# Performance work log

Measured on AMD Instinct MI355X. Metric: run time of the kernel, lower is better.

The kernel has to match this reference:

```python
import jax, jax.numpy as jnp
import numpy as np

N, E, G = 50000, 800000, 64
NODE_IN, EDGE_DIM = 128, 16
H1, C1 = 4, 16            # layer1: 4 heads, 16 ch -> concat 64
H2, C2 = 1, 64            # layer2: 1 head, 64 ch, no concat
OUT = 64


def setup_inputs() -> dict:
    key = jax.random.key(0)
    ks = jax.random.split(key, 20)
    s = 0.05
    inp = {
        "x": jax.random.normal(ks[0], (N, NODE_IN), jnp.float32),
        "edge_index": jax.random.randint(ks[1], (2, E), 0, N, jnp.int32),
        "edge_attr": jax.random.normal(ks[2], (E, EDGE_DIM), jnp.float32),
        "batch": jnp.sort(jax.random.randint(ks[3], (N,), 0, G, jnp.int32)),
        # layer 1 params
        "W1": jax.random.normal(ks[4], (NODE_IN, H1 * C1), jnp.float32) * s,
        "as1": jax.random.normal(ks[5], (H1, C1), jnp.float32) * s,
        "ad1": jax.random.normal(ks[6], (H1, C1), jnp.float32) * s,
        "We1": jax.random.normal(ks[7], (EDGE_DIM, H1 * C1), jnp.float32) * s,
        "ae1": jax.random.normal(ks[8], (H1, C1), jnp.float32) * s,
        "b1": jnp.zeros((H1 * C1,), jnp.float32),
        # layer 2 params
        "W2": jax.random.normal(ks[9], (H1 * C1, H2 * C2), jnp.float32) * s,
        "as2": jax.random.normal(ks[10], (H2, C2), jnp.float32) * s,
        "ad2": jax.random.normal(ks[11], (H2, C2), jnp.float32) * s,
        "We2": jax.random.normal(ks[12], (EDGE_DIM, H2 * C2), jnp.float32) * s,
        "ae2": jax.random.normal(ks[13], (H2, C2), jnp.float32) * s,
        "b2": jnp.zeros((C2,), jnp.float32),
        # final projection
        "Pw": jax.random.normal(ks[14], (OUT, OUT), jnp.float32) * s,
        "Pb": jnp.zeros((OUT,), jnp.float32),
    }
    return inp


def _gat(x, src, dst, edge_attr, W, a_s, a_d, We, a_e, b, heads, ch, concat):
    """PyG GATConv: shared lin, edge features, self-loops with mean fill,
    LeakyReLU(0.2), segment softmax over dst, sum aggregation."""
    n = x.shape[0]
    h = (x @ W).reshape(n, heads, ch)                    # [N,H,C]
    al_s = jnp.einsum("nhc,hc->nh", h, a_s)              # [N,H]
    al_d = jnp.einsum("nhc,hc->nh", h, a_d)
    # add self-loops; loop edge_attr = mean of incoming edge attrs (fill='mean')
    deg = jax.ops.segment_sum(jnp.ones((src.shape[0],), x.dtype), dst, n)
    loop_attr = jax.ops.segment_sum(edge_attr, dst, n) / jnp.maximum(deg, 1.0)[:, None]
    ar = jnp.arange(n, dtype=src.dtype)
    s_idx = jnp.concatenate([src, ar])
    d_idx = jnp.concatenate([dst, ar])
    ea = jnp.concatenate([edge_attr, loop_attr], axis=0)
    al_e = jnp.einsum("ehc,hc->eh", (ea @ We).reshape(-1, heads, ch), a_e)
    alpha = jax.nn.leaky_relu(al_s[s_idx] + al_d[d_idx] + al_e, 0.2)  # [E',H]
    # segment softmax over incoming edges of each dst node
    amax = jax.ops.segment_max(alpha, d_idx, num_segments=n)
    ex = jnp.exp(alpha - amax[d_idx])
    denom = jax.ops.segment_sum(ex, d_idx, num_segments=n)
    att = ex / denom[d_idx]                              # safe: self-loops guarantee denom>0
    msg = h[s_idx] * att[..., None]                      # [E',H,C]
    out = jax.ops.segment_sum(msg.reshape(-1, heads * ch), d_idx, num_segments=n)
    out = out if concat else out.reshape(n, heads, ch).mean(axis=1)
    return out + b


def reference(x, edge_index, edge_attr, batch,
              W1, as1, ad1, We1, ae1, b1,
              W2, as2, ad2, We2, ae2, b2, Pw, Pb):
    src, dst = edge_index[0], edge_index[1]
    h = jax.nn.elu(_gat(x, src, dst, edge_attr, W1, as1, ad1, We1, ae1, b1, H1, C1, True))
    h = _gat(h, src, dst, edge_attr, W2, as2, ad2, We2, ae2, b2, H2, C2, False)
    # global mean pool over graphs
    cnt = jax.ops.segment_sum(jnp.ones((N,), h.dtype), batch, num_segments=G)
    pooled = jax.ops.segment_sum(h, batch, num_segments=G) / jnp.maximum(cnt, 1.0)[:, None]
    return pooled @ Pw + Pb
```

## Files before the change

kernel.cpp:

```cpp
#include <hip/hip_runtime.h>

#define LRELU(a) ((a) > 0.f ? (a) : 0.2f * (a))

__device__ __forceinline__ int blockScanIncl256(int v, int* wl) {
  int t = threadIdx.x, lane = t & 63, w = t >> 6;
  int x = v;
#pragma unroll
  for (int o = 1; o < 64; o <<= 1) {
    int tmp = __shfl_up(x, (unsigned)o, 64);
    if (lane >= o) x += tmp;
  }
  if (lane == 63) wl[w] = x;
  __syncthreads();
  if (t == 0) {
    int s = 0;
#pragma unroll
    for (int j = 0; j < 4; ++j) { int tv = wl[j]; wl[j] = s; s += tv; }
  }
  __syncthreads();
  return x + wl[w];
}

__global__ __launch_bounds__(256) void k_deg(const int* __restrict__ dst,
                                             int* __restrict__ deg, int E) {
  int e = blockIdx.x * 256 + threadIdx.x;
  if (e < E) atomicAdd(&deg[dst[e]], 1);
}

__global__ __launch_bounds__(256) void k_chunksum(const int* __restrict__ deg,
                                                  int* __restrict__ bsum, int n) {
  __shared__ int wl[4];
  int i = blockIdx.x * 256 + threadIdx.x;
  int v = (i < n) ? deg[i] : 0;
#pragma unroll
  for (int o = 1; o < 64; o <<= 1) v += __shfl_xor(v, o, 64);
  int lane = threadIdx.x & 63, w = threadIdx.x >> 6;
  if (lane == 0) wl[w] = v;
  __syncthreads();
  if (threadIdx.x == 0) bsum[blockIdx.x] = wl[0] + wl[1] + wl[2] + wl[3];
}

__global__ __launch_bounds__(256) void k_bscan(int* __restrict__ bsum, int nb,
                                               int* __restrict__ csr_off, int n) {
  __shared__ int wl[4];
  int t = threadIdx.x;
  int v = (t < nb) ? bsum[t] : 0;
  int incl = blockScanIncl256(v, wl);
  if (t < nb) bsum[t] = incl - v;
  if (t == 255) csr_off[n] = incl;
}

__global__ __launch_bounds__(256) void k_chunkscan(const int* __restrict__ deg,
                                                   const int* __restrict__ bsum,
                                                   int* __restrict__ csr_off,
                                                   int* __restrict__ fill, int n) {
  __shared__ int wl[4];
  int i = blockIdx.x * 256 + threadIdx.x;
  int v = (i < n) ? deg[i] : 0;
  int incl = blockScanIncl256(v, wl);
  int o = bsum[blockIdx.x] + incl - v;
  if (i < n) { csr_off[i] = o; fill[i] = o; }
}

template <int K, int HH>
__device__ __forceinline__ void gemm_body(const float* __restrict__ X,
                                          const float* __restrict__ W,
                                          const float* __restrict__ a_s,
                                          const float* __restrict__ a_d,
                                          float* __restrict__ H,
                                          float* __restrict__ als,
                                          float* __restrict__ ald,
                                          int n, int bid) {
  constexpr int KC = 32;
  __shared__ float Xs[64][KC + 4];
  __shared__ float Ws[KC][64 + 4];
  int t = threadIdx.x;
  int b0 = bid * 64;
  int tx = t & 15, ty = t >> 4;
  float acc[4][4] = {};
  for (int kc = 0; kc < K; kc += KC) {
    if (kc) __syncthreads();
    {
      int i = t * 8;
      int node = i >> 5, k = i & 31;
      int r = b0 + node;
      float4 v0 = make_float4(0.f, 0.f, 0.f, 0.f), v1 = v0;
      if (r < n) {
        const float* src = X + (size_t)r * K + kc + k;
        v0 = *(const float4*)src;
        v1 = *(const float4*)(src + 4);
      }
      *(float4*)&Xs[node][k] = v0;
      *(float4*)&Xs[node][k + 4] = v1;
    }
    {
      int i = t * 8;
      int kk = i >> 6, c = i & 63;
      const float* src = W + (size_t)(kc + kk) * 64 + c;
      *(float4*)&Ws[kk][c] = *(const float4*)src;
      *(float4*)&Ws[kk][c + 4] = *(const float4*)(src + 4);
    }
    __syncthreads();
#pragma unroll
    for (int k4 = 0; k4 < KC; k4 += 4) {
      float wvf[4][4];
#pragma unroll
      for (int j = 0; j < 4; ++j)
        *(float4*)&wvf[j][0] = *(const float4*)&Ws[k4 + j][tx * 4];
#pragma unroll
      for (int i = 0; i < 4; ++i) {
        float xvf[4];
        *(float4*)&xvf[0] = *(const float4*)&Xs[ty * 4 + i][k4];
#pragma unroll
        for (int kk = 0; kk < 4; ++kk)
#pragma unroll
          for (int j = 0; j < 4; ++j)
            acc[i][j] = fmaf(xvf[kk], wvf[kk][j], acc[i][j]);
      }
    }
  }
#pragma unroll
  for (int i = 0; i < 4; ++i) {
    int node = b0 + ty * 4 + i;
    if (node < n)
      *(float4*)&H[(size_t)node * 64 + tx * 4] =
          make_float4(acc[i][0], acc[i][1], acc[i][2], acc[i][3]);
  }
  constexpr int C = 64 / HH;
  constexpr int GL = C / 4;
  float asv[4], adv[4];
#pragma unroll
  for (int j = 0; j < 4; ++j) { asv[j] = a_s[tx * 4 + j]; adv[j] = a_d[tx * 4 + j]; }
#pragma unroll
  for (int i = 0; i < 4; ++i) {
    float ps = 0.f, pd = 0.f;
#pragma unroll
    for (int j = 0; j < 4; ++j) {
      ps = fmaf(acc[i][j], asv[j], ps);
      pd = fmaf(acc[i][j], adv[j], pd);
    }
#pragma unroll
    for (int o = 1; o < GL; o <<= 1) {
      ps += __shfl_xor(ps, o, 64);
      pd += __shfl_xor(pd, o, 64);
    }
    int node = b0 + ty * 4 + i;
    if (node < n && (tx & (GL - 1)) == 0) {
      int head = tx / GL;
      als[(size_t)node * HH + head] = ps;
      ald[(size_t)node * HH + head] = pd;
    }
  }
}

__global__ __launch_bounds__(256) void k_gemm2(const float* __restrict__ X,
                                               const float* __restrict__ W,
                                               const float* __restrict__ a_s,
                                               const float* __restrict__ a_d,
                                               float* __restrict__ H,
                                               float* __restrict__ als,
                                               float* __restrict__ ald, int n) {
  gemm_body<64, 1>(X, W, a_s, a_d, H, als, ald, n, blockIdx.x);
}

__global__ __launch_bounds__(256) void k_gs(const float* __restrict__ X,
                                            const float* __restrict__ W,
                                            const float* __restrict__ a_s,
                                            const float* __restrict__ a_d,
                                            float* __restrict__ H,
                                            float* __restrict__ als,
                                            float* __restrict__ ald, int n,
                                            int gemmBlocks,
                                            const int* __restrict__ dst,
                                            const int* __restrict__ src,
                                            const float* __restrict__ edge_attr,
                                            const float* __restrict__ We1,
                                            const float* __restrict__ ae1,
                                            const float* __restrict__ We2,
                                            const float* __restrict__ ae2,
                                            int* __restrict__ fill,
                                            float* __restrict__ epk, int E) {
  if ((int)blockIdx.x < gemmBlocks) {
    gemm_body<128, 4>(X, W, a_s, a_d, H, als, ald, n, blockIdx.x);
  } else {
    __shared__ float wa1s[64];
    __shared__ float wa2s[16];
    int t = threadIdx.x;
    if (t < 64) {
      int k = t >> 2, hh = t & 3;
      float s = 0.f;
#pragma unroll
      for (int c = 0; c < 16; ++c)
        s = fmaf(We1[k * 64 + hh * 16 + c], ae1[hh * 16 + c], s);
      wa1s[t] = s;
    } else if (t < 80) {
      int k = t - 64;
      float s = 0.f;
#pragma unroll
      for (int c = 0; c < 64; ++c) s = fmaf(We2[k * 64 + c], ae2[c], s);
      wa2s[k] = s;
    }
    __syncthreads();
    int base = (blockIdx.x - gemmBlocks) * 512 + t;
#pragma unroll
    for (int r = 0; r < 2; ++r) {
      int e = base + r * 256;
      if (e < E) {
        int d = dst[e], s = src[e];
        const float4* ea = (const float4*)(edge_attr + (size_t)e * 16);
        float ev[16];
        *(float4*)&ev[0]  = ea[0];
        *(float4*)&ev[4]  = ea[1];
        *(float4*)&ev[8]  = ea[2];
        *(float4*)&ev[12] = ea[3];
        float d0 = 0.f, d1 = 0.f, d2 = 0.f, d3 = 0.f, q = 0.f;
#pragma unroll
        for (int k = 0; k < 16; ++k) {
          float4 w1 = *(const float4*)&wa1s[k * 4];
          d0 = fmaf(ev[k], w1.x, d0);
          d1 = fmaf(ev[k], w1.y, d1);
          d2 = fmaf(ev[k], w1.z, d2);
          d3 = fmaf(ev[k], w1.w, d3);
          q  = fmaf(ev[k], wa2s[k], q);
        }
        int p = atomicAdd(&fill[d], 1);
        float* o = epk + (size_t)p * 8;
        *(float4*)o = make_float4(d0, d1, d2, d3);
        *(float4*)(o + 4) = make_float4(q, __int_as_float(s), 0.f, 0.f);
      }
    }
  }
}

__global__ __launch_bounds__(256) void k_agg1(const int* __restrict__ csr_off,
                                              const float* __restrict__ epk,
                                              const float* __restrict__ als1,
                                              const float* __restrict__ ald1,
                                              const float* __restrict__ h1,
                                              const float* __restrict__ b1,
                                              float* __restrict__ out1,
                                              float* __restrict__ loopdot2, int n) {
  int t = threadIdx.x, w = t >> 6, lane = t & 63;
  int node = blockIdx.x * 4 + w;
  if (node >= n) return;
  int s0 = csr_off[node], s1 = csr_off[node + 1];
  int nit = s1 - s0;
  int laneB = lane >> 2, laneH = lane & 3;
  float adv = ald1[(size_t)node * 4 + laneH];
  float m = -3e38f, den = 0.f, sumd = 0.f, sumq = 0.f;
  for (int i = s0 + laneB; i < s1; i += 16) {
    float d = epk[(size_t)i * 8 + laneH];
    int s = __float_as_int(epk[(size_t)i * 8 + 5]);
    float q = epk[(size_t)i * 8 + 4];
    float a = als1[(size_t)s * 4 + laneH] + adv + d;
    a = LRELU(a);
    float nm = fmaxf(m, a);
    den = den * __expf(m - nm) + __expf(a - nm);
    m = nm;
    sumd += d;
    if (laneH == 0) sumq += q;
  }
#pragma unroll
  for (int o = 4; o < 64; o <<= 1) {
    float om = __shfl_xor(m, o, 64);
    float od = __shfl_xor(den, o, 64);
    float nm = fmaxf(m, om);
    den = den * __expf(m - nm) + od * __expf(om - nm);
    m = nm;
    sumd += __shfl_xor(sumd, o, 64);
    sumq += __shfl_xor(sumq, o, 64);
  }
  float cd = fmaxf((float)nit, 1.f);
  float sl = als1[(size_t)node * 4 + laneH] + adv + sumd / cd;
  sl = LRELU(sl);
  {
    float nm = fmaxf(m, sl);
    den = den * __expf(m - nm) + __expf(sl - nm);
    m = nm;
  }
  if (lane == 0) loopdot2[node] = sumq / cd;
  int head = lane >> 4;
  float m_ch = __shfl(m, head, 64);
  float rd_ch = 1.f / __shfl(den, head, 64);
  float sl_ch = __shfl(sl, head, 64);
  float acc = __expf(sl_ch - m_ch) * h1[(size_t)node * 64 + lane];
  float adv_h = __shfl(adv, head, 64);
  if (nit > 0) {
    int nb = (nit + 7) >> 3;
    int laneE = lane & 7, laneB8 = (lane >> 2) & 7;
    int sv; float ev;
    float bufA[8], bufB[8];
    {
      int i1 = min(s0 + laneE, s1 - 1);
      sv = __float_as_int(epk[(size_t)i1 * 8 + 5]);
      int i2 = min(s0 + laneB8, s1 - 1);
      float d = epk[(size_t)i2 * 8 + laneH];
      int se = __float_as_int(epk[(size_t)i2 * 8 + 5]);
      ev = als1[(size_t)se * 4 + laneH] + adv + d;
      ev = LRELU(ev);
    }
#pragma unroll
    for (int j = 0; j < 8; ++j)
      bufA[j] = h1[(size_t)__shfl(sv, j, 64) * 64 + lane];
    for (int b = 0; b < nb; ++b) {
      int svN = 0; float evN = 0.f;
      bool pf = (b + 1 < nb);
      if (pf) {
        int base = s0 + (b + 1) * 8;
        int i1 = min(base + laneE, s1 - 1);
        svN = __float_as_int(epk[(size_t)i1 * 8 + 5]);
        int i2 = min(base + laneB8, s1 - 1);
        float d = epk[(size_t)i2 * 8 + laneH];
        int se = __float_as_int(epk[(size_t)i2 * 8 + 5]);
        evN = als1[(size_t)se * 4 + laneH] + adv + d;
        evN = LRELU(evN);
#pragma unroll
        for (int j = 0; j < 8; ++j)
          bufB[j] = h1[(size_t)__shfl(svN, j, 64) * 64 + lane];
      }
      int rem = nit - b * 8;
#pragma unroll
      for (int j = 0; j < 8; ++j) {
        float aj = __shfl(ev, j * 4 + head, 64);
        float ex = (j < rem) ? __expf(aj - m_ch) : 0.f;
        acc = fmaf(ex, bufA[j], acc);
      }
      if (pf) {
#pragma unroll
        for (int j = 0; j < 8; ++j) bufA[j] = bufB[j];
        sv = svN; ev = evN;
      }
    }
  }
  float r = acc * rd_ch + b1[lane];
  out1[(size_t)node * 64 + lane] = r > 0.f ? r : expm1f(r);
  (void)adv_h;
}

__global__ __launch_bounds__(256) void k_agg2(const int* __restrict__ csr_off,
                                              const float* __restrict__ epk,
                                              const float* __restrict__ als2,
                                              const float* __restrict__ ald2,
                                              const float* __restrict__ loopdot2,
                                              const float* __restrict__ h2,
                                              const float* __restrict__ b2,
                                              float* __restrict__ out2, int n) {
  int t = threadIdx.x, w = t >> 6, lane = t & 63;
  int node = blockIdx.x * 4 + w;
  if (node >= n) return;
  int s0 = csr_off[node], s1 = csr_off[node + 1];
  int nit = s1 - s0;
  float adv = ald2[node];
  float m = -3e38f, den = 0.f;
  for (int i = s0 + lane; i < s1; i += 64) {
    float q = epk[(size_t)i * 8 + 4];
    int s = __float_as_int(epk[(size_t)i * 8 + 5]);
    float a = als2[s] + adv + q;
    a = LRELU(a);
    float nm = fmaxf(m, a);
    den = den * __expf(m - nm) + __expf(a - nm);
    m = nm;
  }
#pragma unroll
  for (int o = 1; o < 64; o <<= 1) {
    float om = __shfl_xor(m, o, 64);
    float od = __shfl_xor(den, o, 64);
    float nm = fmaxf(m, om);
    den = den * __expf(m - nm) + od * __expf(om - nm);
    m = nm;
  }
  float sl = als2[node] + adv + loopdot2[node];
  sl = LRELU(sl);
  {
    float nm = fmaxf(m, sl);
    den = den * __expf(m - nm) + __expf(sl - nm);
    m = nm;
  }
  float rd = 1.f / den;
  float acc = __expf(sl - m) * h2[(size_t)node * 64 + lane];
  if (nit > 0) {
    int nb = (nit + 7) >> 3;
    int laneE = lane & 7;
    int sv; float ev;
    {
      int i1 = min(s0 + laneE, s1 - 1);
      float q = epk[(size_t)i1 * 8 + 4];
      sv = __float_as_int(epk[(size_t)i1 * 8 + 5]);
      ev = LRELU(als2[sv] + adv + q);
    }
    float bufA[8], bufB[8];
#pragma unroll
    for (int j = 0; j < 8; ++j)
      bufA[j] = h2[(size_t)__shfl(sv, j, 64) * 64 + lane];
    for (int b = 0; b < nb; ++b) {
      int svN = 0; float evN = 0.f;
      bool pf = (b + 1 < nb);
      if (pf) {
        int i1 = min(s0 + (b + 1) * 8 + laneE, s1 - 1);
        float q = epk[(size_t)i1 * 8 + 4];
        svN = __float_as_int(epk[(size_t)i1 * 8 + 5]);
        evN = LRELU(als2[svN] + adv + q);
#pragma unroll
        for (int j = 0; j < 8; ++j)
          bufB[j] = h2[(size_t)__shfl(svN, j, 64) * 64 + lane];
      }
      int rem = nit - b * 8;
#pragma unroll
      for (int j = 0; j < 8; ++j) {
        float aj = __shfl(ev, j, 64);
        float ex = (j < rem) ? __expf(aj - m) : 0.f;
        acc = fmaf(ex, bufA[j], acc);
      }
      if (pf) {
#pragma unroll
        for (int j = 0; j < 8; ++j) bufA[j] = bufB[j];
        sv = svN; ev = evN;
      }
    }
  }
  out2[(size_t)node * 64 + lane] = acc * rd + b2[lane];
}

__global__ __launch_bounds__(256) void k_pool(const float* __restrict__ out2,
                                              const int* __restrict__ batch,
                                              float* __restrict__ pooled,
                                              float* __restrict__ cnt, int n) {
  int wgl = blockIdx.x * 4 + (threadIdx.x >> 6);
  int lane = threadIdx.x & 63;
  int i0 = wgl * 64;
  if (i0 >= n) return;
  int i1 = min(i0 + 64, n);
  int cur = -1;
  float acc = 0.f, c = 0.f;
  for (int i = i0; i < i1; ++i) {
    int g = batch[i];
    if (g != cur) {
      if (cur >= 0) {
        atomicAdd(&pooled[cur * 64 + lane], acc);
        if (lane == 0) atomicAdd(&cnt[cur], c);
      }
      cur = g; acc = 0.f; c = 0.f;
    }
    acc += out2[(size_t)i * 64 + lane];
    c += 1.f;
  }
  if (cur >= 0) {
    atomicAdd(&pooled[cur * 64 + lane], acc);
    if (lane == 0) atomicAdd(&cnt[cur], c);
  }
}

__global__ __launch_bounds__(64) void k_final(const float* __restrict__ pooled,
                                              const float* __restrict__ cnt,
                                              const float* __restrict__ Pw,
                                              const float* __restrict__ Pb,
                                              float* __restrict__ out) {
  __shared__ float m[64];
  int g = blockIdx.x, o = threadIdx.x;
  m[o] = pooled[g * 64 + o] / fmaxf(cnt[g], 1.f);
  __syncthreads();
  float s = Pb[o];
#pragma unroll
  for (int c = 0; c < 64; ++c) s = fmaf(m[c], Pw[c * 64 + o], s);
  out[g * 64 + o] = s;
}

extern "C" void kernel_launch(void* const* d_in, const int* in_sizes, int n_in,
                              void* d_out, int out_size, void* d_ws, size_t ws_size,
                              hipStream_t stream) {
  const float* x         = (const float*)d_in[0];
  const int*   edge_index= (const int*)d_in[1];
  const float* edge_attr = (const float*)d_in[2];
  const int*   batch     = (const int*)d_in[3];
  const float* W1  = (const float*)d_in[4];
  const float* as1 = (const float*)d_in[5];
  const float* ad1 = (const float*)d_in[6];
  const float* We1 = (const float*)d_in[7];
  const float* ae1 = (const float*)d_in[8];
  const float* b1  = (const float*)d_in[9];
  const float* W2  = (const float*)d_in[10];
  const float* as2 = (const float*)d_in[11];
  const float* ad2 = (const float*)d_in[12];
  const float* We2 = (const float*)d_in[13];
  const float* ae2 = (const float*)d_in[14];
  const float* b2  = (const float*)d_in[15];
  const float* Pw  = (const float*)d_in[16];
  const float* Pb  = (const float*)d_in[17];

  const int N = in_sizes[0] / 128;
  const int E = in_sizes[1] / 2;
  const int G = out_size / 64;
  const int* srcI = edge_index;
  const int* dstI = edge_index + E;

  float* ws = (float*)d_ws;
  size_t off = 0;
  auto alloc = [&](size_t elems) {
    float* p = ws + off;
    off += (elems + 7) & ~(size_t)7;
    return p;
  };
  int*   deg       = (int*)alloc(N);
  float* cnt       = alloc(G);
  float* pooled    = alloc((size_t)G * 64);
  size_t zero_bytes = off * sizeof(float);
  int*   csr_off   = (int*)alloc(N + 1);
  int*   fill      = (int*)alloc(N);
  int*   bsum      = (int*)alloc(1024);
  float* epk       = alloc((size_t)E * 8);
  float* loopdot2  = alloc((size_t)N);
  float* h         = alloc((size_t)N * 64);
  float* als       = alloc((size_t)N * 4);
  float* ald       = alloc((size_t)N * 4);
  float* outn      = alloc((size_t)N * 64);

  (void)ws_size; (void)n_in;
  hipMemsetAsync(d_ws, 0, zero_bytes, stream);

  const int ebl   = (E + 255) / 256;
  const int nb    = (N + 255) / 256;
  const int nbl4  = (N + 3) / 4;
  const int gemb  = (N + 63) / 64;
  const int sctb  = (E + 511) / 512;

  k_deg<<<ebl, 256, 0, stream>>>(dstI, deg, E);
  k_chunksum<<<nb, 256, 0, stream>>>(deg, bsum, N);
  k_bscan<<<1, 256, 0, stream>>>(bsum, nb, csr_off, N);
  k_chunkscan<<<nb, 256, 0, stream>>>(deg, bsum, csr_off, fill, N);

  k_gs<<<gemb + sctb, 256, 0, stream>>>(x, W1, as1, ad1, h, als, ald, N, gemb,
                                        dstI, srcI, edge_attr, We1, ae1, We2, ae2,
                                        fill, epk, E);

  k_agg1<<<nbl4, 256, 0, stream>>>(csr_off, epk, als, ald, h, b1, outn, loopdot2, N);

  k_gemm2<<<gemb, 256, 0, stream>>>(outn, W2, as2, ad2, h, als, ald, N);
  k_agg2<<<nbl4, 256, 0, stream>>>(csr_off, epk, als, ald, loopdot2, h, b2, outn, N);

  k_pool<<<((N + 63) / 64 + 3) / 4, 256, 0, stream>>>(outn, batch, pooled, cnt, N);
  k_final<<<G, 64, 0, stream>>>(pooled, cnt, Pw, Pb, (float*)d_out);
}
```

Before: 244.1 us.

## Fuse layer-2 linear projection and attention logits into layer-1 aggregation kernel

Layer 1's aggregation kernel now applies ELU, multiplies the 64-wide row by W2 using wavefront shuffles, and writes h2 plus the layer-2 source and destination attention scalars directly. This removes the separate GEMM launch and the round trip of the N x 64 layer-1 output through global memory. It also doubles the edges handled per scatter block and reads the packed q/src pair with a single float2 load in the layer-2 aggregation. In exchange each wavefront runs 64 shuffle-broadcast FMAs that reload W2 from global memory or cache, which adds latency at the tail of the aggregation kernel.

Measured after the change: 261.9 us. 1.07x slower.

```diff
diff --git a/kernel.cpp b/kernel.cpp
--- a/kernel.cpp
+++ b/kernel.cpp
@@ -153,16 +153,6 @@
   }
 }
 
-__global__ __launch_bounds__(256) void k_gemm2(const float* __restrict__ X,
-                                               const float* __restrict__ W,
-                                               const float* __restrict__ a_s,
-                                               const float* __restrict__ a_d,
-                                               float* __restrict__ H,
-                                               float* __restrict__ als,
-                                               float* __restrict__ ald, int n) {
-  gemm_body<64, 1>(X, W, a_s, a_d, H, als, ald, n, blockIdx.x);
-}
-
 __global__ __launch_bounds__(256) void k_gs(const float* __restrict__ X,
                                             const float* __restrict__ W,
                                             const float* __restrict__ a_s,
@@ -201,9 +191,9 @@
       wa2s[k] = s;
     }
     __syncthreads();
-    int base = (blockIdx.x - gemmBlocks) * 512 + t;
-#pragma unroll
-    for (int r = 0; r < 2; ++r) {
+    int base = (blockIdx.x - gemmBlocks) * 1024 + t;
+#pragma unroll
+    for (int r = 0; r < 4; ++r) {
       int e = base + r * 256;
       if (e < E) {
         int d = dst[e], s = src[e];
@@ -238,7 +228,12 @@
                                               const float* __restrict__ ald1,
                                               const float* __restrict__ h1,
                                               const float* __restrict__ b1,
-                                              float* __restrict__ out1,
+                                              const float* __restrict__ W2,
+                                              const float* __restrict__ as2,
+                                              const float* __restrict__ ad2,
+                                              float* __restrict__ h2,
+                                              float* __restrict__ als2,
+                                              float* __restrict__ ald2,
                                               float* __restrict__ loopdot2, int n) {
   int t = threadIdx.x, w = t >> 6, lane = t & 63;
   int node = blockIdx.x * 4 + w;
@@ -284,7 +279,6 @@
   float rd_ch = 1.f / __shfl(den, head, 64);
   float sl_ch = __shfl(sl, head, 64);
   float acc = __expf(sl_ch - m_ch) * h1[(size_t)node * 64 + lane];
-  float adv_h = __shfl(adv, head, 64);
   if (nit > 0) {
     int nb = (nit + 7) >> 3;
     int laneE = lane & 7, laneB8 = (lane >> 2) & 7;
@@ -333,8 +327,28 @@
     }
   }
   float r = acc * rd_ch + b1[lane];
-  out1[(size_t)node * 64 + lane] = r > 0.f ? r : expm1f(r);
-  (void)adv_h;
+  r = r > 0.f ? r : expm1f(r);
+  float a0 = 0.f, a1 = 0.f, a2 = 0.f, a3 = 0.f;
+#pragma unroll
+  for (int k = 0; k < 64; k += 4) {
+    float r0 = __shfl(r, k, 64);
+    float r1 = __shfl(r, k + 1, 64);
+    float r2 = __shfl(r, k + 2, 64);
+    float r3 = __shfl(r, k + 3, 64);
+    a0 = fmaf(r0, W2[(k + 0) * 64 + lane], a0);
+    a1 = fmaf(r1, W2[(k + 1) * 64 + lane], a1);
+    a2 = fmaf(r2, W2[(k + 2) * 64 + lane], a2);
+    a3 = fmaf(r3, W2[(k + 3) * 64 + lane], a3);
+  }
+  float h2v = (a0 + a1) + (a2 + a3);
+  h2[(size_t)node * 64 + lane] = h2v;
+  float ps = h2v * as2[lane], pd = h2v * ad2[lane];
+#pragma unroll
+  for (int o = 1; o < 64; o <<= 1) {
+    ps += __shfl_xor(ps, o, 64);
+    pd += __shfl_xor(pd, o, 64);
+  }
+  if (lane == 0) { als2[node] = ps; ald2[node] = pd; }
 }
 
 __global__ __launch_bounds__(256) void k_agg2(const int* __restrict__ csr_off,
@@ -353,9 +367,9 @@
   float adv = ald2[node];
   float m = -3e38f, den = 0.f;
   for (int i = s0 + lane; i < s1; i += 64) {
-    float q = epk[(size_t)i * 8 + 4];
-    int s = __float_as_int(epk[(size_t)i * 8 + 5]);
-    float a = als2[s] + adv + q;
+    float2 qs = *(const float2*)(epk + (size_t)i * 8 + 4);
+    int s = __float_as_int(qs.y);
+    float a = als2[s] + adv + qs.x;
     a = LRELU(a);
     float nm = fmaxf(m, a);
     den = den * __expf(m - nm) + __expf(a - nm);
@@ -384,9 +398,9 @@
     int sv; float ev;
     {
       int i1 = min(s0 + laneE, s1 - 1);
-      float q = epk[(size_t)i1 * 8 + 4];
-      sv = __float_as_int(epk[(size_t)i1 * 8 + 5]);
-      ev = LRELU(als2[sv] + adv + q);
+      float2 qs = *(const float2*)(epk + (size_t)i1 * 8 + 4);
+      sv = __float_as_int(qs.y);
+      ev = LRELU(als2[sv] + adv + qs.x);
     }
     float bufA[8], bufB[8];
 #pragma unroll
@@ -397,9 +411,9 @@
       bool pf = (b + 1 < nb);
       if (pf) {
         int i1 = min(s0 + (b + 1) * 8 + laneE, s1 - 1);
-        float q = epk[(size_t)i1 * 8 + 4];
-        svN = __float_as_int(epk[(size_t)i1 * 8 + 5]);
-        evN = LRELU(als2[svN] + adv + q);
+        float2 qs = *(const float2*)(epk + (size_t)i1 * 8 + 4);
+        svN = __float_as_int(qs.y);
+        evN = LRELU(als2[svN] + adv + qs.x);
 #pragma unroll
         for (int j = 0; j < 8; ++j)
           bufB[j] = h2[(size_t)__shfl(svN, j, 64) * 64 + lane];
@@ -512,7 +526,9 @@
   float* h         = alloc((size_t)N * 64);
   float* als       = alloc((size_t)N * 4);
   float* ald       = alloc((size_t)N * 4);
-  float* outn      = alloc((size_t)N * 64);
+  float* h2buf     = alloc((size_t)N * 64);
+  float* als2      = alloc((size_t)N);
+  float* ald2      = alloc((size_t)N);
 
   (void)ws_size; (void)n_in;
   hipMemsetAsync(d_ws, 0, zero_bytes, stream);
@@ -521,7 +537,7 @@
   const int nb    = (N + 255) / 256;
   const int nbl4  = (N + 3) / 4;
   const int gemb  = (N + 63) / 64;
-  const int sctb  = (E + 511) / 512;
+  const int sctb  = (E + 1023) / 1024;
 
   k_deg<<<ebl, 256, 0, stream>>>(dstI, deg, E);
   k_chunksum<<<nb, 256, 0, stream>>>(deg, bsum, N);
@@ -532,11 +548,12 @@
                                         dstI, srcI, edge_attr, We1, ae1, We2, ae2,
                                         fill, epk, E);
 
-  k_agg1<<<nbl4, 256, 0, stream>>>(csr_off, epk, als, ald, h, b1, outn, loopdot2, N);
-
-  k_gemm2<<<gemb, 256, 0, stream>>>(outn, W2, as2, ad2, h, als, ald, N);
-  k_agg2<<<nbl4, 256, 0, stream>>>(csr_off, epk, als, ald, loopdot2, h, b2, outn, N);
-
-  k_pool<<<((N + 63) / 64 + 3) / 4, 256, 0, stream>>>(outn, batch, pooled, cnt, N);
+  k_agg1<<<nbl4, 256, 0, stream>>>(csr_off, epk, als, ald, h, b1,
+                                   W2, as2, ad2, h2buf, als2, ald2, loopdot2, N);
+
+  k_agg2<<<nbl4, 256, 0, stream>>>(csr_off, epk, als2, ald2, loopdot2, h2buf, b2,
+                                   h, N);
+
+  k_pool<<<((N + 63) / 64 + 3) / 4, 256, 0, stream>>>(h, batch, pooled, cnt, N);
   k_final<<<G, 64, 0, stream>>>(pooled, cnt, Pw, Pb, (float*)d_out);
 }
```

## Fuse softmax stats pass into aggregation via online softmax in GAT kernels

Applied to the files above, without the earlier changes.

Both aggregation kernels drop the separate first pass over incoming edges that computed the softmax max and denominator. They instead keep a running max, denominator and weighted accumulator that are rescaled per batch of 8 edges, and fold the self-loop in at the end. Layer 1 also accumulates the edge-attribute sums for the self-loop mean inside the same loop. Layer 2 reads the q and src fields as one float2, and the edge-scatter blocks handle 4 edges per thread instead of 2. This removes a second read of the CSR edge data per node, at the cost of extra exp and rescale work per batch.

New measurement: 239.2 us. -2.0%, faster.

```diff
diff --git a/kernel.cpp b/kernel.cpp
--- a/kernel.cpp
+++ b/kernel.cpp
@@ -201,9 +201,9 @@
       wa2s[k] = s;
     }
     __syncthreads();
-    int base = (blockIdx.x - gemmBlocks) * 512 + t;
-#pragma unroll
-    for (int r = 0; r < 2; ++r) {
+    int base = (blockIdx.x - gemmBlocks) * 1024 + t;
+#pragma unroll
+    for (int r = 0; r < 4; ++r) {
       int e = base + r * 256;
       if (e < E) {
         int d = dst[e], s = src[e];
@@ -245,96 +245,88 @@
   if (node >= n) return;
   int s0 = csr_off[node], s1 = csr_off[node + 1];
   int nit = s1 - s0;
-  int laneB = lane >> 2, laneH = lane & 3;
+  int laneH = lane & 3, laneE = lane & 7, laneB8 = (lane >> 2) & 7;
+  int head = lane >> 4;
   float adv = ald1[(size_t)node * 4 + laneH];
-  float m = -3e38f, den = 0.f, sumd = 0.f, sumq = 0.f;
-  for (int i = s0 + laneB; i < s1; i += 16) {
-    float d = epk[(size_t)i * 8 + laneH];
-    int s = __float_as_int(epk[(size_t)i * 8 + 5]);
-    float q = epk[(size_t)i * 8 + 4];
-    float a = als1[(size_t)s * 4 + laneH] + adv + d;
-    a = LRELU(a);
-    float nm = fmaxf(m, a);
-    den = den * __expf(m - nm) + __expf(a - nm);
-    m = nm;
-    sumd += d;
-    if (laneH == 0) sumq += q;
-  }
-#pragma unroll
-  for (int o = 4; o < 64; o <<= 1) {
-    float om = __shfl_xor(m, o, 64);
-    float od = __shfl_xor(den, o, 64);
-    float nm = fmaxf(m, om);
-    den = den * __expf(m - nm) + od * __expf(om - nm);
-    m = nm;
-    sumd += __shfl_xor(sumd, o, 64);
-    sumq += __shfl_xor(sumq, o, 64);
-  }
-  float cd = fmaxf((float)nit, 1.f);
-  float sl = als1[(size_t)node * 4 + laneH] + adv + sumd / cd;
-  sl = LRELU(sl);
-  {
-    float nm = fmaxf(m, sl);
-    den = den * __expf(m - nm) + __expf(sl - nm);
-    m = nm;
-  }
-  if (lane == 0) loopdot2[node] = sumq / cd;
-  int head = lane >> 4;
-  float m_ch = __shfl(m, head, 64);
-  float rd_ch = 1.f / __shfl(den, head, 64);
-  float sl_ch = __shfl(sl, head, 64);
-  float acc = __expf(sl_ch - m_ch) * h1[(size_t)node * 64 + lane];
-  float adv_h = __shfl(adv, head, 64);
+  float m = -3e38f, den = 0.f, acc = 0.f, sumd = 0.f, sumq = 0.f;
   if (nit > 0) {
     int nb = (nit + 7) >> 3;
-    int laneE = lane & 7, laneB8 = (lane >> 2) & 7;
-    int sv; float ev;
+    int sv; float dv, qv, ev;
     float bufA[8], bufB[8];
     {
       int i1 = min(s0 + laneE, s1 - 1);
       sv = __float_as_int(epk[(size_t)i1 * 8 + 5]);
       int i2 = min(s0 + laneB8, s1 - 1);
-      float d = epk[(size_t)i2 * 8 + laneH];
+      dv = epk[(size_t)i2 * 8 + laneH];
+      qv = epk[(size_t)i2 * 8 + 4];
       int se = __float_as_int(epk[(size_t)i2 * 8 + 5]);
-      ev = als1[(size_t)se * 4 + laneH] + adv + d;
-      ev = LRELU(ev);
+      ev = LRELU(als1[(size_t)se * 4 + laneH] + adv + dv);
     }
 #pragma unroll
     for (int j = 0; j < 8; ++j)
       bufA[j] = h1[(size_t)__shfl(sv, j, 64) * 64 + lane];
     for (int b = 0; b < nb; ++b) {
-      int svN = 0; float evN = 0.f;
+      int svN = 0; float dvN = 0.f, qvN = 0.f, evN = 0.f;
       bool pf = (b + 1 < nb);
       if (pf) {
         int base = s0 + (b + 1) * 8;
         int i1 = min(base + laneE, s1 - 1);
         svN = __float_as_int(epk[(size_t)i1 * 8 + 5]);
         int i2 = min(base + laneB8, s1 - 1);
-        float d = epk[(size_t)i2 * 8 + laneH];
+        dvN = epk[(size_t)i2 * 8 + laneH];
+        qvN = epk[(size_t)i2 * 8 + 4];
         int se = __float_as_int(epk[(size_t)i2 * 8 + 5]);
-        evN = als1[(size_t)se * 4 + laneH] + adv + d;
-        evN = LRELU(evN);
+        evN = LRELU(als1[(size_t)se * 4 + laneH] + adv + dvN);
 #pragma unroll
         for (int j = 0; j < 8; ++j)
           bufB[j] = h1[(size_t)__shfl(svN, j, 64) * 64 + lane];
       }
       int rem = nit - b * 8;
+      if (lane < 32 && laneB8 < rem) {
+        sumd += dv;
+        if (laneH == 0) sumq += qv;
+      }
+      float a[8];
+#pragma unroll
+      for (int j = 0; j < 8; ++j)
+        a[j] = (j < rem) ? __shfl(ev, j * 4 + head, 64) : -3e38f;
+      float bm = fmaxf(fmaxf(fmaxf(a[0], a[1]), fmaxf(a[2], a[3])),
+                       fmaxf(fmaxf(a[4], a[5]), fmaxf(a[6], a[7])));
+      float nm = fmaxf(m, bm);
+      float corr = __expf(m - nm);
+      den *= corr;
+      acc *= corr;
 #pragma unroll
       for (int j = 0; j < 8; ++j) {
-        float aj = __shfl(ev, j * 4 + head, 64);
-        float ex = (j < rem) ? __expf(aj - m_ch) : 0.f;
-        acc = fmaf(ex, bufA[j], acc);
-      }
+        float e = __expf(a[j] - nm);
+        den += e;
+        acc = fmaf(e, bufA[j], acc);
+      }
+      m = nm;
       if (pf) {
 #pragma unroll
         for (int j = 0; j < 8; ++j) bufA[j] = bufB[j];
-        sv = svN; ev = evN;
-      }
-    }
-  }
-  float r = acc * rd_ch + b1[lane];
+        sv = svN; dv = dvN; qv = qvN; ev = evN;
+      }
+    }
+  }
+#pragma unroll
+  for (int o = 4; o < 64; o <<= 1) {
+    sumd += __shfl_xor(sumd, o, 64);
+    sumq += __shfl_xor(sumq, o, 64);
+  }
+  float cd = fmaxf((float)nit, 1.f);
+  float sl = als1[(size_t)node * 4 + laneH] + adv + sumd / cd;
+  sl = LRELU(sl);
+  if (lane == 0) loopdot2[node] = sumq / cd;
+  float sl_ch = __shfl(sl, head, 64);
+  float nm = fmaxf(m, sl_ch);
+  float corr = __expf(m - nm);
+  float es = __expf(sl_ch - nm);
+  den = den * corr + es;
+  acc = acc * corr + es * h1[(size_t)node * 64 + lane];
+  float r = acc / den + b1[lane];
   out1[(size_t)node * 64 + lane] = r > 0.f ? r : expm1f(r);
-  (void)adv_h;
 }
 
 __global__ __launch_bounds__(256) void k_agg2(const int* __restrict__ csr_off,
@@ -351,42 +343,16 @@
   int s0 = csr_off[node], s1 = csr_off[node + 1];
   int nit = s1 - s0;
   float adv = ald2[node];
-  float m = -3e38f, den = 0.f;
-  for (int i = s0 + lane; i < s1; i += 64) {
-    float q = epk[(size_t)i * 8 + 4];
-    int s = __float_as_int(epk[(size_t)i * 8 + 5]);
-    float a = als2[s] + adv + q;
-    a = LRELU(a);
-    float nm = fmaxf(m, a);
-    den = den * __expf(m - nm) + __expf(a - nm);
-    m = nm;
-  }
-#pragma unroll
-  for (int o = 1; o < 64; o <<= 1) {
-    float om = __shfl_xor(m, o, 64);
-    float od = __shfl_xor(den, o, 64);
-    float nm = fmaxf(m, om);
-    den = den * __expf(m - nm) + od * __expf(om - nm);
-    m = nm;
-  }
-  float sl = als2[node] + adv + loopdot2[node];
-  sl = LRELU(sl);
-  {
-    float nm = fmaxf(m, sl);
-    den = den * __expf(m - nm) + __expf(sl - nm);
-    m = nm;
-  }
-  float rd = 1.f / den;
-  float acc = __expf(sl - m) * h2[(size_t)node * 64 + lane];
+  float m = -3e38f, den = 0.f, acc = 0.f;
   if (nit > 0) {
     int nb = (nit + 7) >> 3;
     int laneE = lane & 7;
     int sv; float ev;
     {
       int i1 = min(s0 + laneE, s1 - 1);
-      float q = epk[(size_t)i1 * 8 + 4];
-      sv = __float_as_int(epk[(size_t)i1 * 8 + 5]);
-      ev = LRELU(als2[sv] + adv + q);
+      float2 qs = *(const float2*)(epk + (size_t)i1 * 8 + 4);
+      sv = __float_as_int(qs.y);
+      ev = LRELU(als2[sv] + adv + qs.x);
     }
     float bufA[8], bufB[8];
 #pragma unroll
@@ -397,20 +363,31 @@
       bool pf = (b + 1 < nb);
       if (pf) {
         int i1 = min(s0 + (b + 1) * 8 + laneE, s1 - 1);
-        float q = epk[(size_t)i1 * 8 + 4];
-        svN = __float_as_int(epk[(size_t)i1 * 8 + 5]);
-        evN = LRELU(als2[svN] + adv + q);
+        float2 qs = *(const float2*)(epk + (size_t)i1 * 8 + 4);
+        svN = __float_as_int(qs.y);
+        evN = LRELU(als2[svN] + adv + qs.x);
 #pragma unroll
         for (int j = 0; j < 8; ++j)
           bufB[j] = h2[(size_t)__shfl(svN, j, 64) * 64 + lane];
       }
       int rem = nit - b * 8;
+      float a[8];
+#pragma unroll
+      for (int j = 0; j < 8; ++j)
+        a[j] = (j < rem) ? __shfl(ev, j, 64) : -3e38f;
+      float bm = fmaxf(fmaxf(fmaxf(a[0], a[1]), fmaxf(a[2], a[3])),
+                       fmaxf(fmaxf(a[4], a[5]), fmaxf(a[6], a[7])));
+      float nm = fmaxf(m, bm);
+      float corr = __expf(m - nm);
+      den *= corr;
+      acc *= corr;
 #pragma unroll
       for (int j = 0; j < 8; ++j) {
-        float aj = __shfl(ev, j, 64);
-        float ex = (j < rem) ? __expf(aj - m) : 0.f;
-        acc = fmaf(ex, bufA[j], acc);
-      }
+        float e = __expf(a[j] - nm);
+        den += e;
+        acc = fmaf(e, bufA[j], acc);
+      }
+      m = nm;
       if (pf) {
 #pragma unroll
         for (int j = 0; j < 8; ++j) bufA[j] = bufB[j];
@@ -418,7 +395,13 @@
       }
     }
   }
-  out2[(size_t)node * 64 + lane] = acc * rd + b2[lane];
+  float sl = LRELU(als2[node] + adv + loopdot2[node]);
+  float nm = fmaxf(m, sl);
+  float corr = __expf(m - nm);
+  float es = __expf(sl - nm);
+  den = den * corr + es;
+  acc = acc * corr + es * h2[(size_t)node * 64 + lane];
+  out2[(size_t)node * 64 + lane] = acc / den + b2[lane];
 }
 
 __global__ __launch_bounds__(256) void k_pool(const float* __restrict__ out2,
@@ -521,7 +504,7 @@
   const int nb    = (N + 255) / 256;
   const int nbl4  = (N + 3) / 4;
   const int gemb  = (N + 63) / 64;
-  const int sctb  = (E + 511) / 512;
+  const int sctb  = (E + 1023) / 1024;
 
   k_deg<<<ebl, 256, 0, stream>>>(dstI, deg, E);
   k_chunksum<<<nb, 256, 0, stream>>>(deg, bsum, N);
```
